# Performance work log

Measured on AMD Instinct MI355X. Metric: run time of the kernel, lower is better.

## Reference

```python
import jax, jax.numpy as jnp
import numpy as np

N_NODES = 100000
N_EDGES = 1600000
D_IN = 128
D_HID = 128
N_CLS = 40


def setup_inputs() -> dict:
    key = jax.random.key(0)
    ks = jax.random.split(key, 8)
    x = jax.random.normal(ks[0], (N_NODES, D_IN), dtype=jnp.float32)
    edge_index = jax.random.randint(ks[1], (2, N_EDGES), 0, N_NODES, dtype=jnp.int64)
    s = 1.0 / np.sqrt(D_IN)
    W1_l = jax.random.normal(ks[2], (D_IN, D_HID), dtype=jnp.float32) * s
    W1_r = jax.random.normal(ks[3], (D_IN, D_HID), dtype=jnp.float32) * s
    b1 = jnp.zeros((D_HID,), dtype=jnp.float32)
    s2 = 1.0 / np.sqrt(D_HID)
    W2_l = jax.random.normal(ks[4], (D_HID, N_CLS), dtype=jnp.float32) * s2
    W2_r = jax.random.normal(ks[5], (D_HID, N_CLS), dtype=jnp.float32) * s2
    b2 = jnp.zeros((N_CLS,), dtype=jnp.float32)
    return {"x": x, "edge_index": edge_index, "W1_l": W1_l, "W1_r": W1_r,
            "b1": b1, "W2_l": W2_l, "W2_r": W2_r, "b2": b2}


def _sage_conv(x, src, dst, Wl, Wr, b):
    # mean-aggregate neighbor features (PyG SAGEConv, aggr='mean')
    n = x.shape[0]
    agg = jax.ops.segment_sum(x[src], dst, num_segments=n)           # [N, d]
    deg = jax.ops.segment_sum(jnp.ones_like(dst, dtype=x.dtype), dst, num_segments=n)
    mean = agg / jnp.maximum(deg, 1.0)[:, None]
    # lin_l(mean) + bias + lin_r(x_root)  (lin_r has no bias in PyG)
    return mean @ Wl + b + x @ Wr


def reference(x, edge_index, W1_l, W1_r, b1, W2_l, W2_r, b2):
    src, dst = edge_index[0], edge_index[1]
    h = jax.nn.relu(_sage_conv(x, src, dst, W1_l, W1_r, b1))
    # F.dropout(training=...) is identity in eval mode (deterministic reference)
    out = _sage_conv(h, src, dst, W2_l, W2_r, b2)
    return jax.nn.softmax(out, axis=1)
```

## Files before the change

kernel.cpp:

```cpp
#include <hip/hip_runtime.h>

#define DIM 128
#define NCLS 40
#define CPAD 64
#define NBIN 256
#define BINSH 9
#define CHUNK 4096

typedef unsigned short ushort_t;
typedef __attribute__((ext_vector_type(8))) short bf16x8;
typedef __attribute__((ext_vector_type(4))) float f32x4;
typedef __attribute__((ext_vector_type(2))) float f32x2;
typedef __attribute__((ext_vector_type(4))) unsigned uint4a;

__device__ __forceinline__ ushort_t f2b(float f) {
    union { float f; unsigned u; } v; v.f = f;
    unsigned r = v.u + 0x7FFFu + ((v.u >> 16) & 1u);
    return (ushort_t)(r >> 16);
}

__device__ __forceinline__ float b2f(ushort_t b) {
    union { unsigned u; float f; } v; v.u = ((unsigned)b) << 16;
    return v.f;
}

__device__ __forceinline__ void acc_fp8x4(float4& a, int w) {
    f32x2 lo = __builtin_amdgcn_cvt_pk_f32_fp8(w, false);
    f32x2 hi = __builtin_amdgcn_cvt_pk_f32_fp8(w, true);
    a.x += lo.x; a.y += lo.y; a.z += hi.x; a.w += hi.y;
}

__device__ __forceinline__ void acc_pair(float& a, float& b, unsigned u) {
    union { unsigned x; float f; } lo, hi;
    lo.x = u << 16;
    hi.x = u & 0xFFFF0000u;
    a += lo.f;
    b += hi.f;
}

__device__ __forceinline__ void acc_row40(float* lg, uint4a v0, uint4a v1,
                                          uint4a v2, uint4a v3, uint4a v4) {
    acc_pair(lg[0],  lg[1],  v0.x); acc_pair(lg[2],  lg[3],  v0.y);
    acc_pair(lg[4],  lg[5],  v0.z); acc_pair(lg[6],  lg[7],  v0.w);
    acc_pair(lg[8],  lg[9],  v1.x); acc_pair(lg[10], lg[11], v1.y);
    acc_pair(lg[12], lg[13], v1.z); acc_pair(lg[14], lg[15], v1.w);
    acc_pair(lg[16], lg[17], v2.x); acc_pair(lg[18], lg[19], v2.y);
    acc_pair(lg[20], lg[21], v2.z); acc_pair(lg[22], lg[23], v2.w);
    acc_pair(lg[24], lg[25], v3.x); acc_pair(lg[26], lg[27], v3.y);
    acc_pair(lg[28], lg[29], v3.z); acc_pair(lg[30], lg[31], v3.w);
    acc_pair(lg[32], lg[33], v4.x); acc_pair(lg[34], lg[35], v4.y);
    acc_pair(lg[36], lg[37], v4.z); acc_pair(lg[38], lg[39], v4.w);
}

__global__ __launch_bounds__(256) void prep_kernel(
    const float* __restrict__ x, ushort_t* __restrict__ xbf, unsigned* __restrict__ xq,
    const float* __restrict__ W1r, const float* __restrict__ W1l, ushort_t* __restrict__ Wp,
    const float* __restrict__ W2l, ushort_t* __restrict__ Wp2,
    const float* __restrict__ W2r, ushort_t* __restrict__ Wp2r,
    const int* __restrict__ dst, int* __restrict__ binCnt, int E, int n4, int cb)
{
    const int b = blockIdx.x;
    if (b < cb) {
        int i = b * 256 + threadIdx.x;
        if (i >= n4) return;
        f32x4 v = __builtin_nontemporal_load(((const f32x4*)x) + i);
        ushort4 o;
        o.x = f2b(v.x); o.y = f2b(v.y); o.z = f2b(v.z); o.w = f2b(v.w);
        ((ushort4*)xbf)[i] = o;
        int p = __builtin_amdgcn_cvt_pk_fp8_f32(v.x, v.y, 0, false);
        p = __builtin_amdgcn_cvt_pk_fp8_f32(v.z, v.w, p, true);
        xq[i] = (unsigned)p;
    } else if (b < cb + 128) {
        int o = (b - cb) * 256 + threadIdx.x;
        int j    = o & 7;
        int lane = (o >> 3) & 63;
        int t    = (o >> 9) & 7;
        int kc   = o >> 12;
        int k = kc * 32 + (lane >> 4) * 8 + j;
        int nn = t * 16 + (lane & 15);
        float v = (k < DIM) ? W1r[k * DIM + nn] : W1l[(k - DIM) * DIM + nn];
        Wp[o] = f2b(v);
    } else if (b < cb + 152) {
        int o = (b - cb - 128) * 256 + threadIdx.x;
        int j    = o & 7;
        int lane = (o >> 3) & 63;
        int rem  = o >> 9;
        int t    = rem % 3;
        int kc   = rem / 3;
        int k  = kc * 32 + (lane >> 4) * 8 + j;
        int nn = t * 16 + (lane & 15);
        Wp2[o] = (nn < NCLS) ? f2b(W2l[k * NCLS + nn]) : (ushort_t)0;
    } else if (b < cb + 176) {
        int o = (b - cb - 152) * 256 + threadIdx.x;
        int j    = o & 7;
        int lane = (o >> 3) & 63;
        int rem  = o >> 9;
        int t    = rem % 3;
        int kc   = rem / 3;
        int k  = kc * 32 + (lane >> 4) * 8 + j;
        int nn = t * 16 + (lane & 15);
        Wp2r[o] = (nn < NCLS) ? f2b(W2r[k * NCLS + nn]) : (ushort_t)0;
    } else {
        __shared__ int hist[NBIN];
        hist[threadIdx.x] = 0;
        __syncthreads();
        const int nb = (int)gridDim.x - (cb + 176);
        const int bi = b - (cb + 176);
        const int tid = bi * 256 + threadIdx.x;
        const int stride = nb * 256;
        for (int e = tid; e < E; e += stride)
            atomicAdd(&hist[__builtin_nontemporal_load(dst + e) >> BINSH], 1);
        __syncthreads();
        if (hist[threadIdx.x]) atomicAdd(&binCnt[threadIdx.x], hist[threadIdx.x]);
    }
}


__global__ __launch_bounds__(256) void binscatter_kernel(
    const int* __restrict__ src, const int* __restrict__ dst,
    const int* __restrict__ binCnt, int* __restrict__ binCtr,
    unsigned* __restrict__ pairs, int E)
{
    __shared__ int ss[CHUNK];
    __shared__ int sd[CHUNK];
    __shared__ int excl[NBIN];
    __shared__ int hist[NBIN];
    __shared__ int base[NBIN];
    __shared__ int cnt[NBIN];
    const int t = threadIdx.x;
    excl[t] = binCnt[t];
    __syncthreads();
    for (int off = 1; off < NBIN; off <<= 1) {
        int v = (t >= off) ? excl[t - off] : 0;
        __syncthreads();
        excl[t] += v;
        __syncthreads();
    }
    const int mybase = (t == 0) ? 0 : excl[t - 1];
    __syncthreads();
    excl[t] = mybase;
    __syncthreads();
    const int nchunk = (E + CHUNK - 1) / CHUNK;
    for (int c = blockIdx.x; c < nchunk; c += gridDim.x) {
        const int e0 = c * CHUNK;
        const int m = min(CHUNK, E - e0);
        for (int i = t; i < m; i += 256) {
            ss[i] = __builtin_nontemporal_load(src + e0 + i);
            sd[i] = __builtin_nontemporal_load(dst + e0 + i);
        }
        hist[t] = 0;
        cnt[t] = 0;
        __syncthreads();
        for (int i = t; i < m; i += 256)
            atomicAdd(&hist[sd[i] >> BINSH], 1);
        __syncthreads();
        base[t] = hist[t] ? (excl[t] + atomicAdd(&binCtr[t], hist[t])) : 0;
        __syncthreads();
        for (int i = t; i < m; i += 256) {
            int d = sd[i];
            int b = d >> BINSH;
            int off = base[b] + atomicAdd(&cnt[b], 1);
            pairs[off] = ((unsigned)(d & ((1 << BINSH) - 1)) << 17) | (unsigned)ss[i];
        }
        __syncthreads();
    }
}

__global__ __launch_bounds__(256) void bincsr_kernel(
    const unsigned* __restrict__ pairs, const int* __restrict__ binCnt,
    int* __restrict__ row_ptr, int* __restrict__ eidx, int n, int E)
{
    __shared__ int bs[NBIN];
    __shared__ int deg[512];
    __shared__ int sc[512];
    __shared__ int cnt[512];
    const int b  = blockIdx.x;
    const int t = threadIdx.x;
    bs[t] = binCnt[t];
    __syncthreads();
    for (int off = 1; off < NBIN; off <<= 1) {
        int v = (t >= off) ? bs[t - off] : 0;
        __syncthreads();
        bs[t] += v;
        __syncthreads();
    }
    const int lo = (b == 0) ? 0 : bs[b - 1];
    const int hi = bs[b];
    const int nlo = b << BINSH;
    deg[t] = 0; deg[t + 256] = 0;
    cnt[t] = 0; cnt[t + 256] = 0;
    __syncthreads();
    for (int e = lo + t; e < hi; e += 256)
        atomicAdd(&deg[pairs[e] >> 17], 1);
    __syncthreads();
    sc[t] = deg[t];
    sc[t + 256] = deg[t + 256];
    __syncthreads();
    for (int off = 1; off < 512; off <<= 1) {
        int v0 = (t >= off) ? sc[t - off] : 0;
        int v1 = sc[t + 256 - off];
        __syncthreads();
        sc[t] += v0;
        sc[t + 256] += v1;
        __syncthreads();
    }
    {
        int node0 = nlo + t;
        int node1 = nlo + t + 256;
        if (node0 < n) row_ptr[node0] = lo + sc[t] - deg[t];
        if (node1 < n) row_ptr[node1] = lo + sc[t + 256] - deg[t + 256];
    }
    if (b == NBIN - 1 && t == 255) row_ptr[n] = E;
    for (int e = lo + t; e < hi; e += 256) {
        unsigned p = pairs[e];
        int dl = p >> 17;
        int slot = sc[dl] - deg[dl] + atomicAdd(&cnt[dl], 1);
        eidx[lo + slot] = (int)(p & 0x1FFFFu);
    }
}


__global__ __launch_bounds__(256) void gather128_kernel(
    const unsigned* __restrict__ xq, const int* __restrict__ row_ptr,
    const int* __restrict__ eidx, ushort_t* __restrict__ Bbf, int n)
{
    int t = blockIdx.x * 256 + threadIdx.x;
    int node = t >> 5;
    if (node >= n) return;
    int q = t & 31;
    int j  = row_ptr[node];
    int je = row_ptr[node + 1];
    const float id = 1.0f / fmaxf((float)(je - j), 1.0f);
    float4 acc = make_float4(0.f, 0.f, 0.f, 0.f);
    for (; j + 7 < je; j += 8) {
        int s0 = eidx[j],     s1 = eidx[j + 1], s2 = eidx[j + 2], s3 = eidx[j + 3];
        int s4 = eidx[j + 4], s5 = eidx[j + 5], s6 = eidx[j + 6], s7 = eidx[j + 7];
        int w0 = (int)xq[(size_t)s0 * 32 + q];
        int w1 = (int)xq[(size_t)s1 * 32 + q];
        int w2 = (int)xq[(size_t)s2 * 32 + q];
        int w3 = (int)xq[(size_t)s3 * 32 + q];
        int w4 = (int)xq[(size_t)s4 * 32 + q];
        int w5 = (int)xq[(size_t)s5 * 32 + q];
        int w6 = (int)xq[(size_t)s6 * 32 + q];
        int w7 = (int)xq[(size_t)s7 * 32 + q];
        acc_fp8x4(acc, w0); acc_fp8x4(acc, w1);
        acc_fp8x4(acc, w2); acc_fp8x4(acc, w3);
        acc_fp8x4(acc, w4); acc_fp8x4(acc, w5);
        acc_fp8x4(acc, w6); acc_fp8x4(acc, w7);
    }
    for (; j + 3 < je; j += 4) {
        int s0 = eidx[j], s1 = eidx[j + 1], s2 = eidx[j + 2], s3 = eidx[j + 3];
        int w0 = (int)xq[(size_t)s0 * 32 + q];
        int w1 = (int)xq[(size_t)s1 * 32 + q];
        int w2 = (int)xq[(size_t)s2 * 32 + q];
        int w3 = (int)xq[(size_t)s3 * 32 + q];
        acc_fp8x4(acc, w0); acc_fp8x4(acc, w1);
        acc_fp8x4(acc, w2); acc_fp8x4(acc, w3);
    }
    for (; j < je; ++j) {
        int s0 = eidx[j];
        acc_fp8x4(acc, (int)xq[(size_t)s0 * 32 + q]);
    }
    ushort4 o;
    o.x = f2b(acc.x * id); o.y = f2b(acc.y * id);
    o.z = f2b(acc.z * id); o.w = f2b(acc.w * id);
    ((ushort4*)(Bbf + (size_t)node * DIM))[q] = o;
}

__global__ __launch_bounds__(256) void mfma_gemm_kernel(
    const ushort_t* __restrict__ xbf, const ushort_t* __restrict__ mxbf,
    const ushort_t* __restrict__ Wp, const ushort_t* __restrict__ Wp2,
    const ushort_t* __restrict__ Wp2r, const float* __restrict__ bias,
    ushort_t* __restrict__ Cbf, float* __restrict__ Dfl, int n)
{
    __shared__ ushort_t hl[4][16 * 136];
    const int wave = threadIdx.x >> 6;
    const int lane = threadIdx.x & 63;
    const int m16  = lane & 15;
    const int quad = lane >> 4;
    const int row0 = blockIdx.x * 64 + wave * 16;
    int arow = row0 + m16;
    if (arow >= n) arow = n - 1;
    f32x4 acc[8];
    #pragma unroll
    for (int t = 0; t < 8; ++t) acc[t] = (f32x4){0.f, 0.f, 0.f, 0.f};
    const ushort_t* __restrict__ xrow = xbf  + (size_t)arow * DIM;
    const ushort_t* __restrict__ mrow = mxbf + (size_t)arow * DIM;
    #pragma unroll
    for (int kc = 0; kc < 8; ++kc) {
        const int kcol = (kc & 3) * 32 + quad * 8;
        const bf16x8 afrag = *(const bf16x8*)((kc < 4 ? xrow : mrow) + kcol);
        const ushort_t* __restrict__ wp = Wp + (size_t)kc * 4096 + (size_t)lane * 8;
        #pragma unroll
        for (int t = 0; t < 8; ++t) {
            const bf16x8 bfrag = *(const bf16x8*)(wp + (size_t)t * 512);
            acc[t] = __builtin_amdgcn_mfma_f32_16x16x32_bf16(afrag, bfrag, acc[t], 0, 0, 0);
        }
    }
    ushort_t* __restrict__ hw = hl[wave];
    #pragma unroll
    for (int t = 0; t < 8; ++t) {
        const int col = t * 16 + m16;
        const float bv = bias[col];
        #pragma unroll
        for (int r = 0; r < 4; ++r) {
            hw[(quad * 4 + r) * 136 + col] = f2b(fmaxf(acc[t][r] + bv, 0.f));
        }
    }
    f32x4 acc2[3];
    f32x4 acc3[3];
    #pragma unroll
    for (int t = 0; t < 3; ++t) {
        acc2[t] = (f32x4){0.f, 0.f, 0.f, 0.f};
        acc3[t] = (f32x4){0.f, 0.f, 0.f, 0.f};
    }
    #pragma unroll
    for (int kc = 0; kc < 4; ++kc) {
        const bf16x8 afrag2 = *(const bf16x8*)(hw + m16 * 136 + kc * 32 + quad * 8);
        const ushort_t* __restrict__ wp2  = Wp2  + (size_t)kc * 1536 + (size_t)lane * 8;
        const ushort_t* __restrict__ wp2r = Wp2r + (size_t)kc * 1536 + (size_t)lane * 8;
        #pragma unroll
        for (int t = 0; t < 3; ++t) {
            const bf16x8 bfrag  = *(const bf16x8*)(wp2  + (size_t)t * 512);
            const bf16x8 bfragr = *(const bf16x8*)(wp2r + (size_t)t * 512);
            acc2[t] = __builtin_amdgcn_mfma_f32_16x16x32_bf16(afrag2, bfrag,  acc2[t], 0, 0, 0);
            acc3[t] = __builtin_amdgcn_mfma_f32_16x16x32_bf16(afrag2, bfragr, acc3[t], 0, 0, 0);
        }
    }
    #pragma unroll
    for (int t = 0; t < 3; ++t) {
        const int col = t * 16 + m16;
        if (col >= NCLS) continue;
        #pragma unroll
        for (int r = 0; r < 4; ++r) {
            const int row = row0 + quad * 4 + r;
            if (row < n) {
                Cbf[(size_t)row * CPAD + col] = f2b(acc2[t][r]);
                Dfl[(size_t)row * NCLS + col] = acc3[t][r];
            }
        }
    }
}

__global__ __launch_bounds__(256) void final_kernel(
    const float* __restrict__ Dfl, const ushort_t* __restrict__ Cbf,
    const int* __restrict__ row_ptr, const int* __restrict__ eidx,
    const float* __restrict__ b2,
    float* __restrict__ out, int n)
{
    __shared__ float lgs[64][41];
    const int tid  = threadIdx.x;
    const int q    = tid >> 6;
    const int lane = tid & 63;
    const int r    = lane & 3;
    const int na   = q * 16 + (lane >> 2);
    const int nodeA = blockIdx.x * 64 + na;
    float lg[40];
    #pragma unroll
    for (int c = 0; c < 40; ++c) lg[c] = 0.f;
    if (nodeA < n) {
        int j  = row_ptr[nodeA] + r;
        int je = row_ptr[nodeA + 1];
        for (; j + 4 < je; j += 8) {
            int s0 = eidx[j];
            int s1 = eidx[j + 4];
            const uint4a* __restrict__ p0 = (const uint4a*)(Cbf + (size_t)s0 * CPAD);
            const uint4a* __restrict__ p1 = (const uint4a*)(Cbf + (size_t)s1 * CPAD);
            uint4a a0 = p0[0], a1 = p0[1], a2 = p0[2], a3 = p0[3], a4 = p0[4];
            uint4a c0v = p1[0], c1 = p1[1], c2 = p1[2], c3 = p1[3], c4 = p1[4];
            acc_row40(lg, a0, a1, a2, a3, a4);
            acc_row40(lg, c0v, c1, c2, c3, c4);
        }
        if (j < je) {
            const uint4a* __restrict__ p0 = (const uint4a*)(Cbf + (size_t)eidx[j] * CPAD);
            uint4a a0 = p0[0], a1 = p0[1], a2 = p0[2], a3 = p0[3], a4 = p0[4];
            acc_row40(lg, a0, a1, a2, a3, a4);
        }
    }
    const bool hi1 = (lane & 1) != 0;
    float h20[20];
    #pragma unroll
    for (int i = 0; i < 20; ++i) {
        float sendv = hi1 ? lg[i] : lg[20 + i];
        float recv  = __shfl_xor(sendv, 1, 64);
        h20[i] = (hi1 ? lg[20 + i] : lg[i]) + recv;
    }
    const bool hi2 = (lane & 2) != 0;
    float h10[10];
    #pragma unroll
    for (int i = 0; i < 10; ++i) {
        float sendv = hi2 ? h20[i] : h20[10 + i];
        float recv  = __shfl_xor(sendv, 2, 64);
        h10[i] = (hi2 ? h20[10 + i] : h20[i]) + recv;
    }
    const int cbase = (hi1 ? 20 : 0) + (hi2 ? 10 : 0);
    #pragma unroll
    for (int i = 0; i < 10; ++i) lgs[na][cbase + i] = h10[i];
    __syncthreads();
    const int c0 = __builtin_amdgcn_readfirstlane(q * 10);
    const int node = blockIdx.x * 64 + lane;
    if (node < n) {
        const float dg = (float)(row_ptr[node + 1] - row_ptr[node]);
        const float id = 1.0f / fmaxf(dg, 1.0f);
        const float* __restrict__ drow = Dfl + (size_t)node * NCLS + c0;
        #pragma unroll
        for (int c = 0; c < 10; ++c)
            lgs[lane][c0 + c] = fmaf(lgs[lane][c0 + c], id, b2[c0 + c]) + drow[c];
    }
    __syncthreads();
    if (q == 0 && node < n) {
        float v[NCLS];
        #pragma unroll
        for (int c = 0; c < NCLS; ++c) v[c] = lgs[lane][c];
        float m = v[0];
        #pragma unroll
        for (int c = 1; c < NCLS; ++c) m = fmaxf(m, v[c]);
        float s = 0.f;
        #pragma unroll
        for (int c = 0; c < NCLS; ++c) { v[c] = __expf(v[c] - m); s += v[c]; }
        const float inv = 1.0f / s;
        float* __restrict__ o = out + (size_t)node * NCLS;
        #pragma unroll
        for (int c = 0; c < NCLS; ++c) o[c] = v[c] * inv;
    }
}

extern "C" void kernel_launch(void* const* d_in, const int* in_sizes, int n_in,
                              void* d_out, int out_size, void* d_ws, size_t ws_size,
                              hipStream_t stream) {
    const float* x   = (const float*)d_in[0];
    const int*   ei  = (const int*)d_in[1];
    const float* W1l = (const float*)d_in[2];
    const float* W1r = (const float*)d_in[3];
    const float* b1  = (const float*)d_in[4];
    const float* W2l = (const float*)d_in[5];
    const float* W2r = (const float*)d_in[6];
    const float* b2  = (const float*)d_in[7];
    float* out = (float*)d_out;

    const int n = in_sizes[0] / DIM;
    const int E = in_sizes[1] / 2;
    const int* src = ei;
    const int* dst = ei + E;

    ushort_t* xbf     = (ushort_t*)d_ws;
    ushort_t* mxbf    = xbf + (size_t)n * DIM;
    float*    Dfl     = (float*)(mxbf + (size_t)n * DIM);
    ushort_t* Cbf     = (ushort_t*)(Dfl + (size_t)n * NCLS);
    unsigned* xq      = (unsigned*)(Cbf + (size_t)n * CPAD);
    ushort_t* Wp      = (ushort_t*)(xq + (size_t)n * 32);
    ushort_t* Wp2     = Wp + 256 * DIM;
    ushort_t* Wp2r    = Wp2 + 4 * 1536;
    int*      eidx    = (int*)(Wp2r + 4 * 1536);
    unsigned* pairs   = (unsigned*)(eidx + E);
    int*      row_ptr = (int*)(pairs + E);
    int*      binCnt  = row_ptr + (n + 1);

    hipMemsetAsync(binCnt, 0, 2 * NBIN * sizeof(int), stream);

    const int n4 = n * 32;
    const int cb = (n4 + 255) / 256;
    prep_kernel<<<cb + 176 + 256, 256, 0, stream>>>(x, xbf, xq, W1r, W1l, Wp,
                                                    W2l, Wp2, W2r, Wp2r,
                                                    dst, binCnt, E, n4, cb);

    binscatter_kernel<<<512, 256, 0, stream>>>(src, dst, binCnt, binCnt + NBIN, pairs, E);
    bincsr_kernel    <<<NBIN, 256, 0, stream>>>(pairs, binCnt, row_ptr, eidx, n, E);

    {
        long long t = (long long)n * 32;
        gather128_kernel<<<(int)((t + 255) / 256), 256, 0, stream>>>(xq, row_ptr, eidx, mxbf, n);
    }
    mfma_gemm_kernel<<<(n + 63) / 64, 256, 0, stream>>>(xbf, mxbf, Wp, Wp2, Wp2r,
                                                        b1, Cbf, Dfl, n);

    final_kernel<<<(n + 63) / 64, 256, 0, stream>>>(Dfl, Cbf, row_ptr, eidx, b2, out, n);
}
```

Before: 282.8 us.

## Use finer CSR bins and split final aggregation across eight lanes per node

The CSR build now uses 512 bins of 256 nodes instead of 256 bins of 512 nodes. That gives the bincsr pass twice as many blocks and a smaller per-block scan, while the bin-level scans in binscatter and bincsr handle two entries per thread. The final kernel moves to 512-thread blocks with 8 lanes per node instead of 4, which adds one more shuffle-reduction stage to raise memory-level parallelism in the neighbor gather. The cost is more shared-memory bins, more global atomic counters, and a longer reduction tree.

Result: no change. 285.0 us (+0.8%).

```diff
diff --git a/kernel.cpp b/kernel.cpp
--- a/kernel.cpp
+++ b/kernel.cpp
@@ -3,8 +3,8 @@
 #define DIM 128
 #define NCLS 40
 #define CPAD 64
-#define NBIN 256
-#define BINSH 9
+#define NBIN 512
+#define BINSH 8
 #define CHUNK 4096
 
 typedef unsigned short ushort_t;
@@ -102,16 +102,18 @@
         Wp2r[o] = (nn < NCLS) ? f2b(W2r[k * NCLS + nn]) : (ushort_t)0;
     } else {
         __shared__ int hist[NBIN];
-        hist[threadIdx.x] = 0;
+        const int t = threadIdx.x;
+        hist[t] = 0; hist[t + 256] = 0;
         __syncthreads();
         const int nb = (int)gridDim.x - (cb + 176);
         const int bi = b - (cb + 176);
-        const int tid = bi * 256 + threadIdx.x;
+        const int tid = bi * 256 + t;
         const int stride = nb * 256;
         for (int e = tid; e < E; e += stride)
             atomicAdd(&hist[__builtin_nontemporal_load(dst + e) >> BINSH], 1);
         __syncthreads();
-        if (hist[threadIdx.x]) atomicAdd(&binCnt[threadIdx.x], hist[threadIdx.x]);
+        if (hist[t])       atomicAdd(&binCnt[t],       hist[t]);
+        if (hist[t + 256]) atomicAdd(&binCnt[t + 256], hist[t + 256]);
     }
 }
 
@@ -123,22 +125,26 @@
 {
     __shared__ int ss[CHUNK];
     __shared__ int sd[CHUNK];
+    __shared__ int sc[NBIN];
     __shared__ int excl[NBIN];
     __shared__ int hist[NBIN];
     __shared__ int base[NBIN];
     __shared__ int cnt[NBIN];
     const int t = threadIdx.x;
-    excl[t] = binCnt[t];
+    const int d0 = binCnt[t];
+    const int d1 = binCnt[t + 256];
+    sc[t] = d0; sc[t + 256] = d1;
     __syncthreads();
     for (int off = 1; off < NBIN; off <<= 1) {
-        int v = (t >= off) ? excl[t - off] : 0;
-        __syncthreads();
-        excl[t] += v;
-        __syncthreads();
-    }
-    const int mybase = (t == 0) ? 0 : excl[t - 1];
-    __syncthreads();
-    excl[t] = mybase;
+        int v0 = (t >= off) ? sc[t - off] : 0;
+        int v1 = sc[t + 256 - off];
+        __syncthreads();
+        sc[t] += v0;
+        sc[t + 256] += v1;
+        __syncthreads();
+    }
+    excl[t] = sc[t] - d0;
+    excl[t + 256] = sc[t + 256] - d1;
     __syncthreads();
     const int nchunk = (E + CHUNK - 1) / CHUNK;
     for (int c = blockIdx.x; c < nchunk; c += gridDim.x) {
@@ -148,13 +154,16 @@
             ss[i] = __builtin_nontemporal_load(src + e0 + i);
             sd[i] = __builtin_nontemporal_load(dst + e0 + i);
         }
-        hist[t] = 0;
-        cnt[t] = 0;
+        hist[t] = 0; hist[t + 256] = 0;
+        cnt[t] = 0;  cnt[t + 256] = 0;
         __syncthreads();
         for (int i = t; i < m; i += 256)
             atomicAdd(&hist[sd[i] >> BINSH], 1);
         __syncthreads();
-        base[t] = hist[t] ? (excl[t] + atomicAdd(&binCtr[t], hist[t])) : 0;
+        base[t] = hist[t]
+            ? (excl[t] + atomicAdd(&binCtr[t], hist[t])) : 0;
+        base[t + 256] = hist[t + 256]
+            ? (excl[t + 256] + atomicAdd(&binCtr[t + 256], hist[t + 256])) : 0;
         __syncthreads();
         for (int i = t; i < m; i += 256) {
             int d = sd[i];
@@ -171,46 +180,44 @@
     int* __restrict__ row_ptr, int* __restrict__ eidx, int n, int E)
 {
     __shared__ int bs[NBIN];
-    __shared__ int deg[512];
-    __shared__ int sc[512];
-    __shared__ int cnt[512];
+    __shared__ int deg[256];
+    __shared__ int sc[256];
+    __shared__ int cnt[256];
     const int b  = blockIdx.x;
     const int t = threadIdx.x;
-    bs[t] = binCnt[t];
+    const int c0 = binCnt[t];
+    const int c1 = binCnt[t + 256];
+    bs[t] = c0; bs[t + 256] = c1;
     __syncthreads();
     for (int off = 1; off < NBIN; off <<= 1) {
-        int v = (t >= off) ? bs[t - off] : 0;
-        __syncthreads();
-        bs[t] += v;
-        __syncthreads();
-    }
-    const int lo = (b == 0) ? 0 : bs[b - 1];
+        int v0 = (t >= off) ? bs[t - off] : 0;
+        int v1 = bs[t + 256 - off];
+        __syncthreads();
+        bs[t] += v0;
+        bs[t + 256] += v1;
+        __syncthreads();
+    }
     const int hi = bs[b];
+    const int lo = hi - binCnt[b];
     const int nlo = b << BINSH;
-    deg[t] = 0; deg[t + 256] = 0;
-    cnt[t] = 0; cnt[t + 256] = 0;
+    deg[t] = 0; cnt[t] = 0;
     __syncthreads();
     for (int e = lo + t; e < hi; e += 256)
         atomicAdd(&deg[pairs[e] >> 17], 1);
     __syncthreads();
     sc[t] = deg[t];
-    sc[t + 256] = deg[t + 256];
-    __syncthreads();
-    for (int off = 1; off < 512; off <<= 1) {
-        int v0 = (t >= off) ? sc[t - off] : 0;
-        int v1 = sc[t + 256 - off];
-        __syncthreads();
-        sc[t] += v0;
-        sc[t + 256] += v1;
+    __syncthreads();
+    for (int off = 1; off < 256; off <<= 1) {
+        int v = (t >= off) ? sc[t - off] : 0;
+        __syncthreads();
+        sc[t] += v;
         __syncthreads();
     }
     {
         int node0 = nlo + t;
-        int node1 = nlo + t + 256;
         if (node0 < n) row_ptr[node0] = lo + sc[t] - deg[t];
-        if (node1 < n) row_ptr[node1] = lo + sc[t + 256] - deg[t + 256];
-    }
-    if (b == NBIN - 1 && t == 255) row_ptr[n] = E;
+    }
+    if (b == (int)gridDim.x - 1 && t == 255) row_ptr[n] = E;
     for (int e = lo + t; e < hi; e += 256) {
         unsigned p = pairs[e];
         int dl = p >> 17;
@@ -342,7 +349,7 @@
     }
 }
 
-__global__ __launch_bounds__(256) void final_kernel(
+__global__ __launch_bounds__(512) void final_kernel(
     const float* __restrict__ Dfl, const ushort_t* __restrict__ Cbf,
     const int* __restrict__ row_ptr, const int* __restrict__ eidx,
     const float* __restrict__ b2,
@@ -352,8 +359,8 @@
     const int tid  = threadIdx.x;
     const int q    = tid >> 6;
     const int lane = tid & 63;
-    const int r    = lane & 3;
-    const int na   = q * 16 + (lane >> 2);
+    const int r    = lane & 7;
+    const int na   = q * 8 + (lane >> 3);
     const int nodeA = blockIdx.x * 64 + na;
     float lg[40];
     #pragma unroll
@@ -361,9 +368,9 @@
     if (nodeA < n) {
         int j  = row_ptr[nodeA] + r;
         int je = row_ptr[nodeA + 1];
-        for (; j + 4 < je; j += 8) {
+        for (; j + 8 < je; j += 16) {
             int s0 = eidx[j];
-            int s1 = eidx[j + 4];
+            int s1 = eidx[j + 8];
             const uint4a* __restrict__ p0 = (const uint4a*)(Cbf + (size_t)s0 * CPAD);
             const uint4a* __restrict__ p1 = (const uint4a*)(Cbf + (size_t)s1 * CPAD);
             uint4a a0 = p0[0], a1 = p0[1], a2 = p0[2], a3 = p0[3], a4 = p0[4];
@@ -393,18 +400,26 @@
         float recv  = __shfl_xor(sendv, 2, 64);
         h10[i] = (hi2 ? h20[10 + i] : h20[i]) + recv;
     }
-    const int cbase = (hi1 ? 20 : 0) + (hi2 ? 10 : 0);
-    #pragma unroll
-    for (int i = 0; i < 10; ++i) lgs[na][cbase + i] = h10[i];
-    __syncthreads();
-    const int c0 = __builtin_amdgcn_readfirstlane(q * 10);
+    const bool hi3 = (lane & 4) != 0;
+    float h5[5];
+    #pragma unroll
+    for (int i = 0; i < 5; ++i) {
+        float sendv = hi3 ? h10[i] : h10[5 + i];
+        float recv  = __shfl_xor(sendv, 4, 64);
+        h5[i] = (hi3 ? h10[5 + i] : h10[i]) + recv;
+    }
+    const int cbase = (hi1 ? 20 : 0) + (hi2 ? 10 : 0) + (hi3 ? 5 : 0);
+    #pragma unroll
+    for (int i = 0; i < 5; ++i) lgs[na][cbase + i] = h5[i];
+    __syncthreads();
+    const int c0 = __builtin_amdgcn_readfirstlane(q * 5);
     const int node = blockIdx.x * 64 + lane;
     if (node < n) {
         const float dg = (float)(row_ptr[node + 1] - row_ptr[node]);
         const float id = 1.0f / fmaxf(dg, 1.0f);
         const float* __restrict__ drow = Dfl + (size_t)node * NCLS + c0;
         #pragma unroll
-        for (int c = 0; c < 10; ++c)
+        for (int c = 0; c < 5; ++c)
             lgs[lane][c0 + c] = fmaf(lgs[lane][c0 + c], id, b2[c0 + c]) + drow[c];
     }
     __syncthreads();
@@ -474,5 +489,5 @@
     mfma_gemm_kernel<<<(n + 63) / 64, 256, 0, stream>>>(xbf, mxbf, Wp, Wp2, Wp2r,
                                                         b1, Cbf, Dfl, n);
 
-    final_kernel<<<(n + 63) / 64, 256, 0, stream>>>(Dfl, Cbf, row_ptr, eidx, b2, out, n);
-}
+    final_kernel<<<(n + 63) / 64, 512, 0, stream>>>(Dfl, Cbf, row_ptr, eidx, b2, out, n);
+}
```
